# Performance work log

Measured on AMD Instinct MI355X. Metric: run time of the kernel, lower is better.

The kernel has to match this reference:

```python
import jax, jax.numpy as jnp
import numpy as np


def setup_inputs() -> dict:
    key = jax.random.key(0)
    ks = jax.random.split(key, 6)
    N, E, F_IN, H, C = 100000, 800000, 96, 128, 64
    x = jax.random.normal(ks[0], (N, F_IN), dtype=jnp.float32)
    W1 = jax.random.normal(ks[1], (F_IN, H), dtype=jnp.float32) * (1.0 / np.sqrt(F_IN))
    b1 = jnp.zeros((H,), dtype=jnp.float32)
    W2 = jax.random.normal(ks[2], (H, C), dtype=jnp.float32) * (1.0 / np.sqrt(H))
    b2 = jnp.zeros((C,), dtype=jnp.float32)
    edge_index = jax.random.randint(ks[3], (2, E), 0, N, dtype=jnp.int64)
    return {"x": x, "W1": W1, "b1": b1, "W2": W2, "b2": b2, "edge_index": edge_index}


def _gcn_norm(edge_index, num_nodes):
    # Add self-loops, compute symmetric normalization D^-1/2 (A+I) D^-1/2.
    loops = jnp.arange(num_nodes, dtype=edge_index.dtype)
    src = jnp.concatenate([edge_index[0], loops])
    dst = jnp.concatenate([edge_index[1], loops])
    deg = jax.ops.segment_sum(jnp.ones_like(dst, dtype=jnp.float32), dst,
                              num_segments=num_nodes)
    dinv = jnp.where(deg > 0, jax.lax.rsqrt(deg), 0.0)
    norm = dinv[src] * dinv[dst]  # [E+N]
    return src, dst, norm


def _gcn_conv(h, W, b, src, dst, norm, num_nodes):
    h = h @ W                              # [N, out] dense GEMM first (PyG order)
    msg = h[src] * norm[:, None]           # gather + scale, [E+N, out]
    agg = jax.ops.segment_sum(msg, dst, num_segments=num_nodes)
    return agg + b


def reference(x, W1, b1, W2, b2, edge_index):
    N = x.shape[0]
    src, dst, norm = _gcn_norm(edge_index, N)
    h = jax.nn.relu(_gcn_conv(x, W1, b1, src, dst, norm, N))
    embedding = h  # post-ReLU, pre-dropout (dropout inactive at eval)
    out = _gcn_conv(h, W2, b2, src, dst, norm, N)
    return jax.nn.log_softmax(out, axis=1), embedding
```

## Files before the change

kernel.cpp:

```cpp
#include <hip/hip_runtime.h>
#include <hip/hip_bf16.h>

#define NN 100000
#define NE 800000
#define FIN 96
#define FH 128
#define FC 64

#define BLOW 9
#define NBK 196
#define BCAP 5120
#define P1E 4096
#define NB_CVTX ((NN * FIN / 4 + 255) / 256)

typedef unsigned short u16;
typedef unsigned int u32;
typedef __attribute__((ext_vector_type(8))) __bf16 bf16x8;
typedef __attribute__((ext_vector_type(4))) float f32x4;

__device__ __forceinline__ float bf2f(u16 u) {
    u32 x = ((u32)u) << 16;
    return __builtin_bit_cast(float, x);
}
__device__ __forceinline__ u16 f2bf(float f) {
    u32 u = __builtin_bit_cast(u32, f);
    u += 0x7fffu + ((u >> 16) & 1u);
    return (u16)(u >> 16);
}
__device__ __forceinline__ void load8f(const u16* p, float* o) {
    uint4 pk = *(const uint4*)p;
    o[0] = bf2f((u16)pk.x); o[1] = bf2f((u16)(pk.x >> 16));
    o[2] = bf2f((u16)pk.y); o[3] = bf2f((u16)(pk.y >> 16));
    o[4] = bf2f((u16)pk.z); o[5] = bf2f((u16)(pk.z >> 16));
    o[6] = bf2f((u16)pk.w); o[7] = bf2f((u16)(pk.w >> 16));
}
__device__ __forceinline__ void store8bf(u16* p, const float* v) {
    uint4 pk;
    pk.x = (u32)f2bf(v[0]) | ((u32)f2bf(v[1]) << 16);
    pk.y = (u32)f2bf(v[2]) | ((u32)f2bf(v[3]) << 16);
    pk.z = (u32)f2bf(v[4]) | ((u32)f2bf(v[5]) << 16);
    pk.w = (u32)f2bf(v[6]) | ((u32)f2bf(v[7]) << 16);
    *(uint4*)p = pk;
}

__global__ __launch_bounds__(256) void k_prep(const int* __restrict__ srcs,
                                              const int* __restrict__ dsts,
                                              int* __restrict__ bucket_cursor,
                                              u32* __restrict__ bucket_data,
                                              const float* __restrict__ x,
                                              u16* __restrict__ xb,
                                              const float* __restrict__ W1,
                                              const float* __restrict__ W2,
                                              u16* __restrict__ W1t,
                                              u16* __restrict__ W2t) {
    __shared__ int s_hist[256];
    __shared__ int s_base[256];
    __shared__ int s_cur[256];
    __shared__ int s_gbase[256];
    __shared__ u32 s_sorted[P1E];
    __shared__ unsigned char s_bkt[P1E];
    int t = threadIdx.x;
    int blk = blockIdx.x;
    if (blk >= NBK) {
        int cb = blk - NBK;
        if (cb < NB_CVTX) {
            int i = (cb * 256 + t) * 4;
            if (i < NN * FIN) {
                float4 f = *(const float4*)(x + i);
                ushort4 o = {f2bf(f.x), f2bf(f.y), f2bf(f.z), f2bf(f.w)};
                *(ushort4*)(xb + i) = o;
            }
        } else {
            for (int i = t; i < FH * FIN + FC * FH; i += 256) {
                if (i < FH * FIN) {
                    int n = i / FIN, k = i % FIN;
                    W1t[i] = f2bf(W1[k * FH + n]);
                } else {
                    int j = i - FH * FIN;
                    int n = j / FH, k = j % FH;
                    W2t[j] = f2bf(W2[k * FC + n]);
                }
            }
        }
        return;
    }
    int e0 = blk * P1E;
    int n = NE - e0; if (n > P1E) n = P1E;
    s_hist[t] = 0;
    __syncthreads();
    u32 rp[16]; int rb[16];
#pragma unroll
    for (int j = 0; j < 16; j++) {
        int i = j * 256 + t;
        rb[j] = -1;
        if (i < n) {
            int s = srcs[e0 + i], d = dsts[e0 + i];
            int b = d >> BLOW;
            rb[j] = b;
            rp[j] = ((u32)(d & ((1 << BLOW) - 1)) << 17) | (u32)s;
            atomicAdd(&s_hist[b], 1);
        }
    }
    __syncthreads();
    int ct = s_hist[t];
    s_base[t] = ct;
    __syncthreads();
    for (int off = 1; off < 256; off <<= 1) {
        int v = (t >= off) ? s_base[t - off] : 0;
        __syncthreads();
        s_base[t] += v;
        __syncthreads();
    }
    int excl = s_base[t] - ct;
    __syncthreads();
    s_base[t] = excl;
    s_cur[t] = excl;
    if (t < NBK) s_gbase[t] = (ct > 0) ? atomicAdd(&bucket_cursor[t], ct) : 0;
    __syncthreads();
#pragma unroll
    for (int j = 0; j < 16; j++) {
        if (rb[j] >= 0) {
            int r = atomicAdd(&s_cur[rb[j]], 1);
            s_sorted[r] = rp[j];
            s_bkt[r] = (unsigned char)rb[j];
        }
    }
    __syncthreads();
    for (int i = t; i < n; i += 256) {
        int b = s_bkt[i];
        int gpos = s_gbase[b] + (i - s_base[b]);
        if (gpos < BCAP)
            bucket_data[(size_t)b * BCAP + gpos] = s_sorted[i];
    }
}

__global__ __launch_bounds__(256) void k_csr(const int* __restrict__ bucket_cursor,
                                             const u32* __restrict__ bucket_data,
                                             int* __restrict__ row_start,
                                             float* __restrict__ dinv,
                                             int* __restrict__ src_sorted) {
    __shared__ int s_c[256];
    __shared__ int s_cnt[512];
    __shared__ int s_ps[256];
    __shared__ int s_off[512];
    __shared__ int s_cur[512];
    __shared__ u32 s_edges[BCAP];
    int t = threadIdx.x;
    int b = blockIdx.x;
    int nbe = bucket_cursor[b];
    if (nbe > BCAP) nbe = BCAP;
    s_c[t] = (t < NBK) ? bucket_cursor[t] : 0;
    __syncthreads();
    for (int off = 1; off < 256; off <<= 1) {
        int v = (t >= off) ? s_c[t - off] : 0;
        __syncthreads();
        s_c[t] += v;
        __syncthreads();
    }
    int bbase = s_c[b] - nbe;
    s_cnt[t] = 0; s_cnt[t + 256] = 0;
    __syncthreads();
    for (int i = t; i < nbe; i += 256) {
        u32 p = bucket_data[(size_t)b * BCAP + i];
        s_edges[i] = p;
        atomicAdd(&s_cnt[p >> 17], 1);
    }
    __syncthreads();
    int c0 = s_cnt[2 * t], c1 = s_cnt[2 * t + 1];
    s_ps[t] = c0 + c1;
    __syncthreads();
    for (int off = 1; off < 256; off <<= 1) {
        int v = (t >= off) ? s_ps[t - off] : 0;
        __syncthreads();
        s_ps[t] += v;
        __syncthreads();
    }
    int pexcl = s_ps[t] - (c0 + c1);
    s_off[2 * t] = pexcl;          s_cur[2 * t] = pexcl;
    s_off[2 * t + 1] = pexcl + c0; s_cur[2 * t + 1] = pexcl + c0;
    __syncthreads();
#pragma unroll
    for (int k = 0; k < 2; k++) {
        int ld = k * 256 + t;
        int gd = b * 512 + ld;
        if (gd < NN) {
            row_start[gd] = bbase + s_off[ld];
            dinv[gd] = rsqrtf((float)s_cnt[ld] + 1.0f);
        }
    }
    if (b == 0 && t == 0) row_start[NN] = NE;
    for (int i = t; i < nbe; i += 256) {
        u32 p = s_edges[i];
        int d = p >> 17;
        int r = atomicAdd(&s_cur[d], 1);
        src_sorted[bbase + r] = (int)(p & 0x1FFFFu);
    }
}

__global__ void k_agg1(const u16* __restrict__ xb, const float* __restrict__ dinv,
                       const int* __restrict__ row_start, const int* __restrict__ src_sorted,
                       u16* __restrict__ aggx) {
    int tid = blockIdx.x * 256 + threadIdx.x;
    int dst = tid / 12, q = tid % 12;
    if (dst >= NN) return;
    int rs = row_start[dst], re = row_start[dst + 1];
    float dv = dinv[dst];
    float acc[8], v0[8], v1[8];
    load8f(xb + (size_t)dst * FIN + q * 8, acc);
#pragma unroll
    for (int j = 0; j < 8; j++) acc[j] *= dv;
    int e = rs;
    for (; e + 1 < re; e += 2) {
        int s0 = src_sorted[e], s1 = src_sorted[e + 1];
        float d0 = dinv[s0], d1 = dinv[s1];
        load8f(xb + (size_t)s0 * FIN + q * 8, v0);
        load8f(xb + (size_t)s1 * FIN + q * 8, v1);
#pragma unroll
        for (int j = 0; j < 8; j++) acc[j] += v0[j] * d0 + v1[j] * d1;
    }
    if (e < re) {
        int s0 = src_sorted[e];
        float d0 = dinv[s0];
        load8f(xb + (size_t)s0 * FIN + q * 8, v0);
#pragma unroll
        for (int j = 0; j < 8; j++) acc[j] += v0[j] * d0;
    }
#pragma unroll
    for (int j = 0; j < 8; j++) acc[j] *= dv;
    store8bf(aggx + (size_t)dst * FIN + q * 8, acc);
}

#define LDSW 136
__global__ __launch_bounds__(128) void k_gemm12(const u16* __restrict__ aggx,
                                                const u16* __restrict__ W1t,
                                                const float* __restrict__ b1,
                                                const u16* __restrict__ W2t,
                                                float* __restrict__ emb,
                                                u16* __restrict__ zb) {
    __shared__ u16 sh[2][16 * LDSW];
    int wid = threadIdx.x >> 6, lane = threadIdx.x & 63;
    int wave = blockIdx.x * 2 + wid;
    int row0 = wave << 4;
    int m = lane & 15, quad = lane >> 4;
    f32x4 acc[8] = {{0,0,0,0},{0,0,0,0},{0,0,0,0},{0,0,0,0},
                    {0,0,0,0},{0,0,0,0},{0,0,0,0},{0,0,0,0}};
#pragma unroll
    for (int kt = 0; kt < 3; kt++) {
        bf16x8 a = *(const bf16x8*)(const void*)(aggx + (size_t)(row0 + m) * FIN + kt * 32 + quad * 8);
#pragma unroll
        for (int nt = 0; nt < 8; nt++) {
            bf16x8 b = *(const bf16x8*)(const void*)(W1t + (size_t)(nt * 16 + m) * FIN + kt * 32 + quad * 8);
            acc[nt] = __builtin_amdgcn_mfma_f32_16x16x32_bf16(a, b, acc[nt], 0, 0, 0);
        }
    }
    u16* tile = sh[wid];
#pragma unroll
    for (int nt = 0; nt < 8; nt++) {
        int c = nt * 16 + m;
        float bias = b1[c];
#pragma unroll
        for (int i = 0; i < 4; i++) {
            int r = quad * 4 + i;
            float val = acc[nt][i] + bias;
            val = val > 0.0f ? val : 0.0f;
            emb[(size_t)(row0 + r) * FH + c] = val;
            tile[r * LDSW + c] = f2bf(val);
        }
    }
    __syncthreads();
    f32x4 zacc[4] = {{0,0,0,0},{0,0,0,0},{0,0,0,0},{0,0,0,0}};
#pragma unroll
    for (int kt = 0; kt < 4; kt++) {
        bf16x8 a = *(const bf16x8*)(const void*)(tile + m * LDSW + kt * 32 + quad * 8);
#pragma unroll
        for (int nt = 0; nt < 4; nt++) {
            bf16x8 b = *(const bf16x8*)(const void*)(W2t + (size_t)(nt * 16 + m) * FH + kt * 32 + quad * 8);
            zacc[nt] = __builtin_amdgcn_mfma_f32_16x16x32_bf16(a, b, zacc[nt], 0, 0, 0);
        }
    }
#pragma unroll
    for (int nt = 0; nt < 4; nt++) {
        int c = nt * 16 + m;
#pragma unroll
        for (int i = 0; i < 4; i++) {
            int r = row0 + quad * 4 + i;
            zb[(size_t)r * FC + c] = f2bf(zacc[nt][i]);
        }
    }
}

__global__ void k_agg2lsm(const u16* __restrict__ zb, const float* __restrict__ dinv,
                          const int* __restrict__ row_start, const int* __restrict__ src_sorted,
                          const float* __restrict__ b2, float* __restrict__ logits) {
    int tid = blockIdx.x * 256 + threadIdx.x;
    int dst = tid >> 3, q = tid & 7;
    if (dst >= NN) return;
    int rs = row_start[dst], re = row_start[dst + 1];
    float dv = dinv[dst];
    float acc[8], v0[8], v1[8];
    load8f(zb + (size_t)dst * FC + q * 8, acc);
#pragma unroll
    for (int j = 0; j < 8; j++) acc[j] *= dv;
    int e = rs;
    for (; e + 1 < re; e += 2) {
        int s0 = src_sorted[e], s1 = src_sorted[e + 1];
        float d0 = dinv[s0], d1 = dinv[s1];
        load8f(zb + (size_t)s0 * FC + q * 8, v0);
        load8f(zb + (size_t)s1 * FC + q * 8, v1);
#pragma unroll
        for (int j = 0; j < 8; j++) acc[j] += v0[j] * d0 + v1[j] * d1;
    }
    if (e < re) {
        int s0 = src_sorted[e];
        float d0 = dinv[s0];
        load8f(zb + (size_t)s0 * FC + q * 8, v0);
#pragma unroll
        for (int j = 0; j < 8; j++) acc[j] += v0[j] * d0;
    }
#pragma unroll
    for (int j = 0; j < 8; j++) acc[j] = acc[j] * dv + b2[q * 8 + j];
    float mx = acc[0];
#pragma unroll
    for (int j = 1; j < 8; j++) mx = fmaxf(mx, acc[j]);
#pragma unroll
    for (int d = 1; d < 8; d <<= 1) mx = fmaxf(mx, __shfl_xor(mx, d, 64));
    float s = 0.0f;
#pragma unroll
    for (int j = 0; j < 8; j++) s += expf(acc[j] - mx);
#pragma unroll
    for (int d = 1; d < 8; d <<= 1) s += __shfl_xor(s, d, 64);
    float lse = mx + logf(s);
    float4 o0 = {acc[0] - lse, acc[1] - lse, acc[2] - lse, acc[3] - lse};
    float4 o1 = {acc[4] - lse, acc[5] - lse, acc[6] - lse, acc[7] - lse};
    *(float4*)(logits + (size_t)dst * FC + q * 8) = o0;
    *(float4*)(logits + (size_t)dst * FC + q * 8 + 4) = o1;
}

extern "C" void kernel_launch(void* const* d_in, const int* in_sizes, int n_in,
                              void* d_out, int out_size, void* d_ws, size_t ws_size,
                              hipStream_t stream) {
    const float* x  = (const float*)d_in[0];
    const float* W1 = (const float*)d_in[1];
    const float* b1 = (const float*)d_in[2];
    const float* W2 = (const float*)d_in[3];
    const float* b2 = (const float*)d_in[4];
    const int* ei   = (const int*)d_in[5];
    const int* srcs = ei;
    const int* dsts = ei + NE;

    float* logits = (float*)d_out;
    float* emb    = (float*)d_out + (size_t)NN * FC;

    char* w = (char*)d_ws;
    float* dinv       = (float*)w; w += 400000;
    int*   row_start  = (int*)w;   w += 400128;
    int*   src_sorted = (int*)w;   w += 3200000;
    int*   bucket_cursor = (int*)w; w += 1024;
    u16*   xb         = (u16*)w;   w += 19200000;
    u16*   aggx       = (u16*)w;   w += 19200000;
    u16*   W1t        = (u16*)w;   w += 24576;
    u16*   W2t        = (u16*)w;   w += 16384;
    u16*   zb         = (u16*)w;   w += 12800000;
    u32*   bucket_data = (u32*)aggx;

    hipMemsetAsync(bucket_cursor, 0, NBK * 4, stream);
    k_prep<<<NBK + NB_CVTX + 1, 256, 0, stream>>>(srcs, dsts, bucket_cursor, bucket_data,
                                                  x, xb, W1, W2, W1t, W2t);
    k_csr<<<NBK, 256, 0, stream>>>(bucket_cursor, bucket_data, row_start, dinv, src_sorted);
    k_agg1<<<(NN * 12 + 255) / 256, 256, 0, stream>>>(xb, dinv, row_start, src_sorted, aggx);
    k_gemm12<<<NN / 32, 128, 0, stream>>>(aggx, W1t, b1, W2t, emb, zb);
    k_agg2lsm<<<(NN * 8 + 255) / 256, 256, 0, stream>>>(zb, dinv, row_start, src_sorted, b2, logits);
}
```

Measured before the change: 224.7 us.

## Pre-scale source features by dinv to drop per-edge dinv gathers

The source-side D^-1/2 scaling moves out of the aggregation loops. k_csr rescales xb in place by dinv, and k_gemm12 multiplies z by dinv before storing zb, so both aggregation kernels just sum neighbor rows and apply the destination dinv once. This removes a dependent random dinv[src] load per edge, and the gather loop is unrolled to four edges for more memory-level parallelism. The cost is an extra read/write pass over xb inside k_csr, an extra bf16 rounding of the pre-scaled features, and the x conversion now handles 8 elements per thread.

```diff
diff --git a/kernel.cpp b/kernel.cpp
--- a/kernel.cpp
+++ b/kernel.cpp
@@ -11,7 +11,7 @@
 #define NBK 196
 #define BCAP 5120
 #define P1E 4096
-#define NB_CVTX ((NN * FIN / 4 + 255) / 256)
+#define NB_CVTX ((NN * FIN / 8 + 255) / 256)
 
 typedef unsigned short u16;
 typedef unsigned int u32;
@@ -64,11 +64,14 @@
     if (blk >= NBK) {
         int cb = blk - NBK;
         if (cb < NB_CVTX) {
-            int i = (cb * 256 + t) * 4;
+            int i = (cb * 256 + t) * 8;
             if (i < NN * FIN) {
-                float4 f = *(const float4*)(x + i);
-                ushort4 o = {f2bf(f.x), f2bf(f.y), f2bf(f.z), f2bf(f.w)};
-                *(ushort4*)(xb + i) = o;
+                float4 f0 = *(const float4*)(x + i);
+                float4 f1 = *(const float4*)(x + i + 4);
+                ushort4 o0 = {f2bf(f0.x), f2bf(f0.y), f2bf(f0.z), f2bf(f0.w)};
+                ushort4 o1 = {f2bf(f1.x), f2bf(f1.y), f2bf(f1.z), f2bf(f1.w)};
+                *(ushort4*)(xb + i) = o0;
+                *(ushort4*)(xb + i + 4) = o1;
             }
         } else {
             for (int i = t; i < FH * FIN + FC * FH; i += 256) {
@@ -138,12 +141,14 @@
                                              const u32* __restrict__ bucket_data,
                                              int* __restrict__ row_start,
                                              float* __restrict__ dinv,
-                                             int* __restrict__ src_sorted) {
+                                             int* __restrict__ src_sorted,
+                                             u16* __restrict__ xb) {
     __shared__ int s_c[256];
     __shared__ int s_cnt[512];
     __shared__ int s_ps[256];
     __shared__ int s_off[512];
     __shared__ int s_cur[512];
+    __shared__ float s_dinv[512];
     __shared__ u32 s_edges[BCAP];
     int t = threadIdx.x;
     int b = blockIdx.x;
@@ -184,16 +189,32 @@
         int ld = k * 256 + t;
         int gd = b * 512 + ld;
         if (gd < NN) {
+            float dv = rsqrtf((float)s_cnt[ld] + 1.0f);
             row_start[gd] = bbase + s_off[ld];
-            dinv[gd] = rsqrtf((float)s_cnt[ld] + 1.0f);
+            dinv[gd] = dv;
+            s_dinv[ld] = dv;
         }
     }
     if (b == 0 && t == 0) row_start[NN] = NE;
+    __syncthreads();
     for (int i = t; i < nbe; i += 256) {
         u32 p = s_edges[i];
         int d = p >> 17;
         int r = atomicAdd(&s_cur[d], 1);
         src_sorted[bbase + r] = (int)(p & 0x1FFFFu);
+    }
+    for (int i = t; i < 512 * 12; i += 256) {
+        int r = i / 12, c = i % 12;
+        int gd = b * 512 + r;
+        if (gd < NN) {
+            float dv = s_dinv[r];
+            float v[8];
+            u16* p = xb + (size_t)gd * FIN + c * 8;
+            load8f(p, v);
+#pragma unroll
+            for (int j = 0; j < 8; j++) v[j] *= dv;
+            store8bf(p, v);
+        }
     }
 }
 
@@ -205,25 +226,24 @@
     if (dst >= NN) return;
     int rs = row_start[dst], re = row_start[dst + 1];
     float dv = dinv[dst];
-    float acc[8], v0[8], v1[8];
+    float acc[8], v0[8], v1[8], v2[8], v3[8];
     load8f(xb + (size_t)dst * FIN + q * 8, acc);
-#pragma unroll
-    for (int j = 0; j < 8; j++) acc[j] *= dv;
     int e = rs;
-    for (; e + 1 < re; e += 2) {
+    for (; e + 3 < re; e += 4) {
         int s0 = src_sorted[e], s1 = src_sorted[e + 1];
-        float d0 = dinv[s0], d1 = dinv[s1];
+        int s2 = src_sorted[e + 2], s3 = src_sorted[e + 3];
         load8f(xb + (size_t)s0 * FIN + q * 8, v0);
         load8f(xb + (size_t)s1 * FIN + q * 8, v1);
-#pragma unroll
-        for (int j = 0; j < 8; j++) acc[j] += v0[j] * d0 + v1[j] * d1;
-    }
-    if (e < re) {
+        load8f(xb + (size_t)s2 * FIN + q * 8, v2);
+        load8f(xb + (size_t)s3 * FIN + q * 8, v3);
+#pragma unroll
+        for (int j = 0; j < 8; j++) acc[j] += (v0[j] + v1[j]) + (v2[j] + v3[j]);
+    }
+    for (; e < re; e++) {
         int s0 = src_sorted[e];
-        float d0 = dinv[s0];
         load8f(xb + (size_t)s0 * FIN + q * 8, v0);
 #pragma unroll
-        for (int j = 0; j < 8; j++) acc[j] += v0[j] * d0;
+        for (int j = 0; j < 8; j++) acc[j] += v0[j];
     }
 #pragma unroll
     for (int j = 0; j < 8; j++) acc[j] *= dv;
@@ -235,6 +255,7 @@
                                                 const u16* __restrict__ W1t,
                                                 const float* __restrict__ b1,
                                                 const u16* __restrict__ W2t,
+                                                const float* __restrict__ dinv,
                                                 float* __restrict__ emb,
                                                 u16* __restrict__ zb) {
     __shared__ u16 sh[2][16 * LDSW];
@@ -267,6 +288,9 @@
             tile[r * LDSW + c] = f2bf(val);
         }
     }
+    float dvr[4];
+#pragma unroll
+    for (int i = 0; i < 4; i++) dvr[i] = dinv[row0 + quad * 4 + i];
     __syncthreads();
     f32x4 zacc[4] = {{0,0,0,0},{0,0,0,0},{0,0,0,0},{0,0,0,0}};
 #pragma unroll
@@ -284,7 +308,7 @@
 #pragma unroll
         for (int i = 0; i < 4; i++) {
             int r = row0 + quad * 4 + i;
-            zb[(size_t)r * FC + c] = f2bf(zacc[nt][i]);
+            zb[(size_t)r * FC + c] = f2bf(zacc[nt][i] * dvr[i]);
         }
     }
 }
@@ -297,25 +321,24 @@
     if (dst >= NN) return;
     int rs = row_start[dst], re = row_start[dst + 1];
     float dv = dinv[dst];
-    float acc[8], v0[8], v1[8];
+    float acc[8], v0[8], v1[8], v2[8], v3[8];
     load8f(zb + (size_t)dst * FC + q * 8, acc);
-#pragma unroll
-    for (int j = 0; j < 8; j++) acc[j] *= dv;
     int e = rs;
-    for (; e + 1 < re; e += 2) {
+    for (; e + 3 < re; e += 4) {
         int s0 = src_sorted[e], s1 = src_sorted[e + 1];
-        float d0 = dinv[s0], d1 = dinv[s1];
+        int s2 = src_sorted[e + 2], s3 = src_sorted[e + 3];
         load8f(zb + (size_t)s0 * FC + q * 8, v0);
         load8f(zb + (size_t)s1 * FC + q * 8, v1);
-#pragma unroll
-        for (int j = 0; j < 8; j++) acc[j] += v0[j] * d0 + v1[j] * d1;
-    }
-    if (e < re) {
+        load8f(zb + (size_t)s2 * FC + q * 8, v2);
+        load8f(zb + (size_t)s3 * FC + q * 8, v3);
+#pragma unroll
+        for (int j = 0; j < 8; j++) acc[j] += (v0[j] + v1[j]) + (v2[j] + v3[j]);
+    }
+    for (; e < re; e++) {
         int s0 = src_sorted[e];
-        float d0 = dinv[s0];
         load8f(zb + (size_t)s0 * FC + q * 8, v0);
 #pragma unroll
-        for (int j = 0; j < 8; j++) acc[j] += v0[j] * d0;
+        for (int j = 0; j < 8; j++) acc[j] += v0[j];
     }
 #pragma unroll
     for (int j = 0; j < 8; j++) acc[j] = acc[j] * dv + b2[q * 8 + j];
@@ -366,8 +389,8 @@
     hipMemsetAsync(bucket_cursor, 0, NBK * 4, stream);
     k_prep<<<NBK + NB_CVTX + 1, 256, 0, stream>>>(srcs, dsts, bucket_cursor, bucket_data,
                                                   x, xb, W1, W2, W1t, W2t);
-    k_csr<<<NBK, 256, 0, stream>>>(bucket_cursor, bucket_data, row_start, dinv, src_sorted);
+    k_csr<<<NBK, 256, 0, stream>>>(bucket_cursor, bucket_data, row_start, dinv, src_sorted, xb);
     k_agg1<<<(NN * 12 + 255) / 256, 256, 0, stream>>>(xb, dinv, row_start, src_sorted, aggx);
-    k_gemm12<<<NN / 32, 128, 0, stream>>>(aggx, W1t, b1, W2t, emb, zb);
+    k_gemm12<<<NN / 32, 128, 0, stream>>>(aggx, W1t, b1, W2t, dinv, emb, zb);
     k_agg2lsm<<<(NN * 8 + 255) / 256, 256, 0, stream>>>(zb, dinv, row_start, src_sorted, b2, logits);
 }
```

New measurement: 229.2 us. +2.0%, slower.

## Fuse layer-1 aggregation into GEMM kernel and pre-scale layer-2 features by source norm

Applied to the files above, without the earlier changes.

Layer-1 neighbor aggregation now runs inside the GEMM kernel and writes its result to shared memory, so the aggx intermediate no longer makes a round trip through global memory and one launch is dropped. The GEMM epilogue multiplies z by dinv of its own row, so the layer-2 aggregation can skip the per-edge dinv gather and unrolls by 4. Bucket data gets its own workspace region, the x conversion handles 8 elements per thread, and a __syncthreads is added in k_csr. The trade-off is that the fused kernel has only 128 threads per block doing irregular gathers, which may lower occupancy and latency hiding for the aggregation step.

```diff
diff --git a/kernel.cpp b/kernel.cpp
--- a/kernel.cpp
+++ b/kernel.cpp
@@ -11,7 +11,7 @@
 #define NBK 196
 #define BCAP 5120
 #define P1E 4096
-#define NB_CVTX ((NN * FIN / 4 + 255) / 256)
+#define NB_CVTX ((NN * FIN / 8 + 255) / 256)
 
 typedef unsigned short u16;
 typedef unsigned int u32;
@@ -64,11 +64,14 @@
     if (blk >= NBK) {
         int cb = blk - NBK;
         if (cb < NB_CVTX) {
-            int i = (cb * 256 + t) * 4;
+            int i = (cb * 256 + t) * 8;
             if (i < NN * FIN) {
-                float4 f = *(const float4*)(x + i);
-                ushort4 o = {f2bf(f.x), f2bf(f.y), f2bf(f.z), f2bf(f.w)};
-                *(ushort4*)(xb + i) = o;
+                float4 f0 = *(const float4*)(x + i);
+                float4 f1 = *(const float4*)(x + i + 4);
+                ushort4 o0 = {f2bf(f0.x), f2bf(f0.y), f2bf(f0.z), f2bf(f0.w)};
+                ushort4 o1 = {f2bf(f1.x), f2bf(f1.y), f2bf(f1.z), f2bf(f1.w)};
+                *(ushort4*)(xb + i) = o0;
+                *(ushort4*)(xb + i + 4) = o1;
             }
         } else {
             for (int i = t; i < FH * FIN + FC * FH; i += 256) {
@@ -189,6 +192,7 @@
         }
     }
     if (b == 0 && t == 0) row_start[NN] = NE;
+    __syncthreads();
     for (int i = t; i < nbe; i += 256) {
         u32 p = s_edges[i];
         int d = p >> 17;
@@ -197,63 +201,67 @@
     }
 }
 
-__global__ void k_agg1(const u16* __restrict__ xb, const float* __restrict__ dinv,
-                       const int* __restrict__ row_start, const int* __restrict__ src_sorted,
-                       u16* __restrict__ aggx) {
-    int tid = blockIdx.x * 256 + threadIdx.x;
-    int dst = tid / 12, q = tid % 12;
-    if (dst >= NN) return;
-    int rs = row_start[dst], re = row_start[dst + 1];
-    float dv = dinv[dst];
-    float acc[8], v0[8], v1[8];
-    load8f(xb + (size_t)dst * FIN + q * 8, acc);
-#pragma unroll
-    for (int j = 0; j < 8; j++) acc[j] *= dv;
-    int e = rs;
-    for (; e + 1 < re; e += 2) {
-        int s0 = src_sorted[e], s1 = src_sorted[e + 1];
-        float d0 = dinv[s0], d1 = dinv[s1];
-        load8f(xb + (size_t)s0 * FIN + q * 8, v0);
-        load8f(xb + (size_t)s1 * FIN + q * 8, v1);
-#pragma unroll
-        for (int j = 0; j < 8; j++) acc[j] += v0[j] * d0 + v1[j] * d1;
-    }
-    if (e < re) {
-        int s0 = src_sorted[e];
-        float d0 = dinv[s0];
-        load8f(xb + (size_t)s0 * FIN + q * 8, v0);
-#pragma unroll
-        for (int j = 0; j < 8; j++) acc[j] += v0[j] * d0;
-    }
-#pragma unroll
-    for (int j = 0; j < 8; j++) acc[j] *= dv;
-    store8bf(aggx + (size_t)dst * FIN + q * 8, acc);
-}
-
+#define ATW 104
 #define LDSW 136
-__global__ __launch_bounds__(128) void k_gemm12(const u16* __restrict__ aggx,
-                                                const u16* __restrict__ W1t,
-                                                const float* __restrict__ b1,
-                                                const u16* __restrict__ W2t,
-                                                float* __restrict__ emb,
-                                                u16* __restrict__ zb) {
-    __shared__ u16 sh[2][16 * LDSW];
-    int wid = threadIdx.x >> 6, lane = threadIdx.x & 63;
-    int wave = blockIdx.x * 2 + wid;
-    int row0 = wave << 4;
+__global__ __launch_bounds__(128) void k_ag1gemm(const u16* __restrict__ xb,
+                                                 const float* __restrict__ dinv,
+                                                 const int* __restrict__ row_start,
+                                                 const int* __restrict__ src_sorted,
+                                                 const u16* __restrict__ W1t,
+                                                 const float* __restrict__ b1,
+                                                 const u16* __restrict__ W2t,
+                                                 float* __restrict__ emb,
+                                                 u16* __restrict__ zb) {
+    __shared__ u16 atile[2][16 * ATW];
+    __shared__ u16 htile[2][16 * LDSW];
+    int t = threadIdx.x;
+    int wid = t >> 6, lane = t & 63;
+    int row0 = blockIdx.x << 5;
+    for (int it = t; it < 384; it += 128) {
+        int dl = it / 12, q = it % 12;
+        int dst = row0 + dl;
+        int rs = row_start[dst], re = row_start[dst + 1];
+        float dv = dinv[dst];
+        float acc[8], v0[8], v1[8];
+        load8f(xb + (size_t)dst * FIN + q * 8, acc);
+#pragma unroll
+        for (int j = 0; j < 8; j++) acc[j] *= dv;
+        int e = rs;
+        for (; e + 1 < re; e += 2) {
+            int s0 = src_sorted[e], s1 = src_sorted[e + 1];
+            float d0 = dinv[s0], d1 = dinv[s1];
+            load8f(xb + (size_t)s0 * FIN + q * 8, v0);
+            load8f(xb + (size_t)s1 * FIN + q * 8, v1);
+#pragma unroll
+            for (int j = 0; j < 8; j++) acc[j] += v0[j] * d0 + v1[j] * d1;
+        }
+        if (e < re) {
+            int s0 = src_sorted[e];
+            float d0 = dinv[s0];
+            load8f(xb + (size_t)s0 * FIN + q * 8, v0);
+#pragma unroll
+            for (int j = 0; j < 8; j++) acc[j] += v0[j] * d0;
+        }
+#pragma unroll
+        for (int j = 0; j < 8; j++) acc[j] *= dv;
+        store8bf(&atile[dl >> 4][(dl & 15) * ATW + q * 8], acc);
+    }
+    __syncthreads();
     int m = lane & 15, quad = lane >> 4;
+    int wrow0 = row0 + (wid << 4);
+    const u16* at = atile[wid];
     f32x4 acc[8] = {{0,0,0,0},{0,0,0,0},{0,0,0,0},{0,0,0,0},
                     {0,0,0,0},{0,0,0,0},{0,0,0,0},{0,0,0,0}};
 #pragma unroll
     for (int kt = 0; kt < 3; kt++) {
-        bf16x8 a = *(const bf16x8*)(const void*)(aggx + (size_t)(row0 + m) * FIN + kt * 32 + quad * 8);
+        bf16x8 a = *(const bf16x8*)(const void*)(at + m * ATW + kt * 32 + quad * 8);
 #pragma unroll
         for (int nt = 0; nt < 8; nt++) {
             bf16x8 b = *(const bf16x8*)(const void*)(W1t + (size_t)(nt * 16 + m) * FIN + kt * 32 + quad * 8);
             acc[nt] = __builtin_amdgcn_mfma_f32_16x16x32_bf16(a, b, acc[nt], 0, 0, 0);
         }
     }
-    u16* tile = sh[wid];
+    u16* tile = htile[wid];
 #pragma unroll
     for (int nt = 0; nt < 8; nt++) {
         int c = nt * 16 + m;
@@ -263,10 +271,13 @@
             int r = quad * 4 + i;
             float val = acc[nt][i] + bias;
             val = val > 0.0f ? val : 0.0f;
-            emb[(size_t)(row0 + r) * FH + c] = val;
+            emb[(size_t)(wrow0 + r) * FH + c] = val;
             tile[r * LDSW + c] = f2bf(val);
         }
     }
+    float dvr[4];
+#pragma unroll
+    for (int i = 0; i < 4; i++) dvr[i] = dinv[wrow0 + quad * 4 + i];
     __syncthreads();
     f32x4 zacc[4] = {{0,0,0,0},{0,0,0,0},{0,0,0,0},{0,0,0,0}};
 #pragma unroll
@@ -283,8 +294,8 @@
         int c = nt * 16 + m;
 #pragma unroll
         for (int i = 0; i < 4; i++) {
-            int r = row0 + quad * 4 + i;
-            zb[(size_t)r * FC + c] = f2bf(zacc[nt][i]);
+            int r = wrow0 + quad * 4 + i;
+            zb[(size_t)r * FC + c] = f2bf(zacc[nt][i] * dvr[i]);
         }
     }
 }
@@ -297,25 +308,24 @@
     if (dst >= NN) return;
     int rs = row_start[dst], re = row_start[dst + 1];
     float dv = dinv[dst];
-    float acc[8], v0[8], v1[8];
+    float acc[8], v0[8], v1[8], v2[8], v3[8];
     load8f(zb + (size_t)dst * FC + q * 8, acc);
-#pragma unroll
-    for (int j = 0; j < 8; j++) acc[j] *= dv;
     int e = rs;
-    for (; e + 1 < re; e += 2) {
+    for (; e + 3 < re; e += 4) {
         int s0 = src_sorted[e], s1 = src_sorted[e + 1];
-        float d0 = dinv[s0], d1 = dinv[s1];
+        int s2 = src_sorted[e + 2], s3 = src_sorted[e + 3];
         load8f(zb + (size_t)s0 * FC + q * 8, v0);
         load8f(zb + (size_t)s1 * FC + q * 8, v1);
-#pragma unroll
-        for (int j = 0; j < 8; j++) acc[j] += v0[j] * d0 + v1[j] * d1;
-    }
-    if (e < re) {
+        load8f(zb + (size_t)s2 * FC + q * 8, v2);
+        load8f(zb + (size_t)s3 * FC + q * 8, v3);
+#pragma unroll
+        for (int j = 0; j < 8; j++) acc[j] += (v0[j] + v1[j]) + (v2[j] + v3[j]);
+    }
+    for (; e < re; e++) {
         int s0 = src_sorted[e];
-        float d0 = dinv[s0];
         load8f(zb + (size_t)s0 * FC + q * 8, v0);
 #pragma unroll
-        for (int j = 0; j < 8; j++) acc[j] += v0[j] * d0;
+        for (int j = 0; j < 8; j++) acc[j] += v0[j];
     }
 #pragma unroll
     for (int j = 0; j < 8; j++) acc[j] = acc[j] * dv + b2[q * 8 + j];
@@ -357,17 +367,16 @@
     int*   src_sorted = (int*)w;   w += 3200000;
     int*   bucket_cursor = (int*)w; w += 1024;
     u16*   xb         = (u16*)w;   w += 19200000;
-    u16*   aggx       = (u16*)w;   w += 19200000;
     u16*   W1t        = (u16*)w;   w += 24576;
     u16*   W2t        = (u16*)w;   w += 16384;
     u16*   zb         = (u16*)w;   w += 12800000;
-    u32*   bucket_data = (u32*)aggx;
+    u16*   bdws       = (u16*)w;   w += 4014080;
+    u32*   bucket_data = (u32*)bdws;
 
     hipMemsetAsync(bucket_cursor, 0, NBK * 4, stream);
     k_prep<<<NBK + NB_CVTX + 1, 256, 0, stream>>>(srcs, dsts, bucket_cursor, bucket_data,
                                                   x, xb, W1, W2, W1t, W2t);
     k_csr<<<NBK, 256, 0, stream>>>(bucket_cursor, bucket_data, row_start, dinv, src_sorted);
-    k_agg1<<<(NN * 12 + 255) / 256, 256, 0, stream>>>(xb, dinv, row_start, src_sorted, aggx);
-    k_gemm12<<<NN / 32, 128, 0, stream>>>(aggx, W1t, b1, W2t, emb, zb);
+    k_ag1gemm<<<NN / 32, 128, 0, stream>>>(xb, dinv, row_start, src_sorted, W1t, b1, W2t, emb, zb);
     k_agg2lsm<<<(NN * 8 + 255) / 256, 256, 0, stream>>>(zb, dinv, row_start, src_sorted, b2, logits);
 }
```

After: 227.5 us. About the same (+1.2%).
